# Optimization experiments

Hardware: AMD Instinct MI355X
Metric: run time of the kernel (lower is better)

## Reference

```python
import jax, jax.numpy as jnp
import numpy as np
import math

D_MODEL = 512
NUM_HEADS = 8
HEAD_DIM = D_MODEL // NUM_HEADS
B, S = 4, 2048


def setup_inputs() -> dict:
    key = jax.random.key(0)
    ks = jax.random.split(key, 11)
    scale = 1.0 / math.sqrt(D_MODEL)
    inp = {
        "Q": jax.random.normal(ks[0], (B, S, D_MODEL), jnp.float32),
        "K": jax.random.normal(ks[1], (B, S, D_MODEL), jnp.float32),
        "V": jax.random.normal(ks[2], (B, S, D_MODEL), jnp.float32),
        # causal mask, broadcast over batch and heads: [1,1,S,S]
        "mask": jnp.tril(jnp.ones((S, S), dtype=bool))[None, None],
        "w_q": jax.random.normal(ks[3], (D_MODEL, D_MODEL), jnp.float32) * scale,
        "b_q": jnp.zeros((D_MODEL,), jnp.float32),
        "w_k": jax.random.normal(ks[4], (D_MODEL, D_MODEL), jnp.float32) * scale,
        "b_k": jnp.zeros((D_MODEL,), jnp.float32),
        "w_v": jax.random.normal(ks[5], (D_MODEL, D_MODEL), jnp.float32) * scale,
        "b_v": jnp.zeros((D_MODEL,), jnp.float32),
        "w_o": jax.random.normal(ks[6], (D_MODEL, D_MODEL), jnp.float32) * scale,
        "b_o": jnp.zeros((D_MODEL,), jnp.float32),
    }
    return inp


def _split_heads(x):
    b, s, _ = x.shape
    return x.reshape(b, s, NUM_HEADS, HEAD_DIM).transpose(0, 2, 1, 3)  # [B,H,S,Dh]


def reference(Q, K, V, mask, w_q, b_q, w_k, b_k, w_v, b_v, w_o, b_o):
    # Linear projections (torch Linear: x @ W.T + b)
    q = _split_heads(Q @ w_q.T + b_q)
    k = _split_heads(K @ w_k.T + b_k)
    v = _split_heads(V @ w_v.T + b_v)

    scores = jnp.einsum("bhqd,bhkd->bhqk", q, k) / math.sqrt(HEAD_DIM)
    scores = jnp.where(mask, scores, -jnp.inf)
    attention = jax.nn.softmax(scores, axis=-1)  # [B,H,S,S]
    ctx = jnp.einsum("bhqk,bhkd->bhqd", attention, v)

    b, h, s, dh = ctx.shape
    x = ctx.transpose(0, 2, 1, 3).reshape(b, s, D_MODEL)
    x = x @ w_o.T + b_o
    return (x, attention)
```

## Files before the change

kernel.cpp:

```cpp
#include <hip/hip_runtime.h>


#define BATCH 4
#define SEQ   2048
#define DM    512
#define NH    8
#define DH    64
#define ROWS  (BATCH*SEQ)
#define QT    (SEQ/64)

typedef unsigned short u16;
using bf8   = __attribute__((ext_vector_type(8))) short;
using f32x4 = __attribute__((ext_vector_type(4))) float;

__device__ __forceinline__ u16 f2b(float f) {
    union { float fl; unsigned int i; } v; v.fl = f;
    return (u16)((v.i + 0x7FFFu + ((v.i >> 16) & 1u)) >> 16);
}

__device__ __forceinline__ void proj_body_f32_bf16(
    const float* __restrict__ Xg, const float* __restrict__ W,
    const float* __restrict__ bias, u16* __restrict__ Cg,
    int row0, int col0)
{
    __shared__ u16 Xs[128][40];
    __shared__ u16 Wsh[128][40];
    const int tid  = threadIdx.x;
    const int lane = tid & 63;
    const int w    = tid >> 6;
    const int wm = (w >> 1) * 64, wn = (w & 1) * 64;
    const int lc = lane & 15, lq = lane >> 4;

    const f32x4 fzero = {0.f, 0.f, 0.f, 0.f};
    f32x4 acc[4][4];
    #pragma unroll
    for (int mt = 0; mt < 4; ++mt)
        #pragma unroll
        for (int nt = 0; nt < 4; ++nt) acc[mt][nt] = fzero;

    for (int k0 = 0; k0 < DM; k0 += 32) {
        __syncthreads();
        {
            const int r = tid >> 3, kc = (tid & 7) * 4;
            #pragma unroll
            for (int rr = 0; rr < 4; ++rr) {
                float4 vx = *(const float4*)(Xg + (size_t)(row0 + r + rr*32) * DM + k0 + kc);
                u16 t4[4] = { f2b(vx.x), f2b(vx.y), f2b(vx.z), f2b(vx.w) };
                *(uint2*)&Xs[r + rr*32][kc] = *(uint2*)t4;
                float4 vw = *(const float4*)(W + (size_t)(col0 + r + rr*32) * DM + k0 + kc);
                u16 t5[4] = { f2b(vw.x), f2b(vw.y), f2b(vw.z), f2b(vw.w) };
                *(uint2*)&Wsh[r + rr*32][kc] = *(uint2*)t5;
            }
        }
        __syncthreads();
        bf8 a[4], b[4];
        #pragma unroll
        for (int mt = 0; mt < 4; ++mt) a[mt] = *(const bf8*)&Xs[wm + mt*16 + lc][lq*8];
        #pragma unroll
        for (int nt = 0; nt < 4; ++nt) b[nt] = *(const bf8*)&Wsh[wn + nt*16 + lc][lq*8];
        __builtin_amdgcn_s_setprio(1);
        #pragma unroll
        for (int mt = 0; mt < 4; ++mt)
            #pragma unroll
            for (int nt = 0; nt < 4; ++nt)
                acc[mt][nt] = __builtin_amdgcn_mfma_f32_16x16x32_bf16(a[mt], b[nt], acc[mt][nt], 0, 0, 0);
        __builtin_amdgcn_s_setprio(0);
    }
    #pragma unroll
    for (int nt = 0; nt < 4; ++nt) {
        const int col = col0 + wn + nt*16 + lc;
        const float bv = bias[col];
        #pragma unroll
        for (int mt = 0; mt < 4; ++mt) {
            #pragma unroll
            for (int r = 0; r < 4; ++r) {
                const int row = row0 + wm + mt*16 + lq*4 + r;
                Cg[(size_t)row * DM + col] = f2b(acc[mt][nt][r] + bv);
            }
        }
    }
}

__global__ __launch_bounds__(256) void proj_qkv(
    const float* __restrict__ Q, const float* __restrict__ K, const float* __restrict__ V,
    const float* __restrict__ wq, const float* __restrict__ wk, const float* __restrict__ wv,
    const float* __restrict__ bq, const float* __restrict__ bk, const float* __restrict__ bv,
    u16* __restrict__ qo, u16* __restrict__ ko, u16* __restrict__ vo)
{
    const int z = blockIdx.z;
    const float* X = (z == 0) ? Q : (z == 1) ? K : V;
    const float* W = (z == 0) ? wq : (z == 1) ? wk : wv;
    const float* B = (z == 0) ? bq : (z == 1) ? bk : bv;
    u16*         C = (z == 0) ? qo : (z == 1) ? ko : vo;
    proj_body_f32_bf16(X, W, B, C, blockIdx.y * 128, blockIdx.x * 128);
}

__global__ __launch_bounds__(256) void proj_out(
    const u16* __restrict__ Xg, const float* __restrict__ W,
    const float* __restrict__ bias, float* __restrict__ Cg)
{
    __shared__ u16 Xs[128][40];
    __shared__ u16 Wsh[128][40];
    const int tid  = threadIdx.x;
    const int lane = tid & 63;
    const int w    = tid >> 6;
    const int wm = (w >> 1) * 64, wn = (w & 1) * 64;
    const int lc = lane & 15, lq = lane >> 4;
    const int row0 = blockIdx.y * 128;
    const int col0 = blockIdx.x * 128;

    const f32x4 fzero = {0.f, 0.f, 0.f, 0.f};
    f32x4 acc[4][4];
    #pragma unroll
    for (int mt = 0; mt < 4; ++mt)
        #pragma unroll
        for (int nt = 0; nt < 4; ++nt) acc[mt][nt] = fzero;

    for (int k0 = 0; k0 < DM; k0 += 32) {
        __syncthreads();
        {
            const u16* Xp = Xg;
            const int r = tid >> 2, kc = (tid & 3) * 8;
            #pragma unroll
            for (int rr = 0; rr < 2; ++rr)
                *(bf8*)&Xs[r + rr*64][kc] =
                    *(const bf8*)(Xp + (size_t)(row0 + r + rr*64) * DM + k0 + kc);
        }
        {
            const int r = tid >> 3, kc = (tid & 7) * 4;
            #pragma unroll
            for (int rr = 0; rr < 4; ++rr) {
                float4 vw = *(const float4*)(W + (size_t)(col0 + r + rr*32) * DM + k0 + kc);
                u16 t4[4] = { f2b(vw.x), f2b(vw.y), f2b(vw.z), f2b(vw.w) };
                *(uint2*)&Wsh[r + rr*32][kc] = *(uint2*)t4;
            }
        }
        __syncthreads();
        bf8 a[4], b[4];
        #pragma unroll
        for (int mt = 0; mt < 4; ++mt) a[mt] = *(const bf8*)&Xs[wm + mt*16 + lc][lq*8];
        #pragma unroll
        for (int nt = 0; nt < 4; ++nt) b[nt] = *(const bf8*)&Wsh[wn + nt*16 + lc][lq*8];
        __builtin_amdgcn_s_setprio(1);
        #pragma unroll
        for (int mt = 0; mt < 4; ++mt)
            #pragma unroll
            for (int nt = 0; nt < 4; ++nt)
                acc[mt][nt] = __builtin_amdgcn_mfma_f32_16x16x32_bf16(a[mt], b[nt], acc[mt][nt], 0, 0, 0);
        __builtin_amdgcn_s_setprio(0);
    }
    #pragma unroll
    for (int nt = 0; nt < 4; ++nt) {
        const int col = col0 + wn + nt*16 + lc;
        const float bv = bias[col];
        #pragma unroll
        for (int mt = 0; mt < 4; ++mt) {
            #pragma unroll
            for (int r = 0; r < 4; ++r) {
                const int row = row0 + wm + mt*16 + lq*4 + r;
                Cg[(size_t)row * DM + col] = acc[mt][nt][r] + bv;
            }
        }
    }
}

__global__ __launch_bounds__(256, 3) void attn_fused(
    const u16* __restrict__ q, const u16* __restrict__ k, const u16* __restrict__ v,
    float* __restrict__ att, u16* __restrict__ ctx)
{
    __shared__ u16 Qs[64][72];
    __shared__ u16 Ks[2][64][72];
    __shared__ u16 Vt[64][72];
    __shared__ u16 Ps[64][72];
    __shared__ float Ls[64][17];
    __shared__ float Lv[64];

    const int tid = threadIdx.x, lane = tid & 63, w = tid >> 6;
    const int lc = lane & 15, lq = lane >> 4;

    const int lin = blockIdx.x + 32 * (blockIdx.y + 8 * blockIdx.z);
    const int xcd = lin & 7, c = lin >> 3;
    const int bh  = xcd * 4 + (c >> 5);
    const int qt  = (QT - 1) - (c & 31);
    const int h = bh & 7, b = bh >> 3;

    const size_t base = ((size_t)b * SEQ) * DM + h * DH;
    const size_t attbase = ((size_t)(b * NH + h)) * SEQ * SEQ;
    const int sr = tid >> 3, sc = (tid & 7) * 8;
    const int dv = tid & 63, jg = (tid >> 6) * 16;
    const f32x4 fzero = {0.f, 0.f, 0.f, 0.f};

    #pragma unroll
    for (int rr = 0; rr < 2; ++rr)
        *(bf8*)&Qs[sr + rr*32][sc] =
            *(const bf8*)(q + base + (size_t)(qt*64 + sr + rr*32) * DM + sc);

    float l_p[4];
    #pragma unroll
    for (int r = 0; r < 4; ++r) l_p[r] = 0.f;

    bf8 kr[2];
    #pragma unroll
    for (int rr = 0; rr < 2; ++rr)
        kr[rr] = *(const bf8*)(k + base + (size_t)(sr + rr*32) * DM + sc);
    #pragma unroll
    for (int rr = 0; rr < 2; ++rr)
        *(bf8*)&Ks[0][sr + rr*32][sc] = kr[rr];

    int cur = 0;
    for (int kt = 0; kt <= qt; ++kt) {
        __syncthreads();
        if (kt < qt) {
            #pragma unroll
            for (int rr = 0; rr < 2; ++rr)
                kr[rr] = *(const bf8*)(k + base + (size_t)((kt+1)*64 + sr + rr*32) * DM + sc);
        }
        f32x4 s[4];
        #pragma unroll
        for (int nt = 0; nt < 4; ++nt) s[nt] = fzero;
        __builtin_amdgcn_s_setprio(1);
        #pragma unroll
        for (int ks = 0; ks < 2; ++ks) {
            bf8 a = *(const bf8*)&Qs[w*16 + lc][ks*32 + lq*8];
            #pragma unroll
            for (int nt = 0; nt < 4; ++nt) {
                bf8 bb = *(const bf8*)&Ks[cur][nt*16 + lc][ks*32 + lq*8];
                s[nt] = __builtin_amdgcn_mfma_f32_16x16x32_bf16(a, bb, s[nt], 0, 0, 0);
            }
        }
        __builtin_amdgcn_s_setprio(0);
        const bool diag = (kt == qt);
        #pragma unroll
        for (int r = 0; r < 4; ++r) {
            const int rowl = w*16 + lq*4 + r;
            float e0, e1, e2, e3;
            {
                float x0 = s[0][r] * 0.125f, x1 = s[1][r] * 0.125f;
                float x2 = s[2][r] * 0.125f, x3 = s[3][r] * 0.125f;
                if (diag) {
                    if ( 0*16 + lc > rowl) x0 = -1e30f;
                    if ( 1*16 + lc > rowl) x1 = -1e30f;
                    if ( 2*16 + lc > rowl) x2 = -1e30f;
                    if ( 3*16 + lc > rowl) x3 = -1e30f;
                }
                e0 = __expf(x0); e1 = __expf(x1); e2 = __expf(x2); e3 = __expf(x3);
            }
            l_p[r] += (e0 + e1) + (e2 + e3);
        }
        if (kt < qt) {
            #pragma unroll
            for (int rr = 0; rr < 2; ++rr)
                *(bf8*)&Ks[cur^1][sr + rr*32][sc] = kr[rr];
        }
        cur ^= 1;
    }

    #pragma unroll
    for (int r = 0; r < 4; ++r)
        Ls[w*16 + lq*4 + r][lc] = l_p[r];
    #pragma unroll
    for (int rr = 0; rr < 2; ++rr)
        kr[rr] = *(const bf8*)(k + base + (size_t)(sr + rr*32) * DM + sc);
    u16 tv[16];
    #pragma unroll
    for (int i = 0; i < 16; ++i)
        tv[i] = v[base + (size_t)(jg + i) * DM + dv];
    __syncthreads();
    if (tid < 64) {
        float lf = 0.f;
        #pragma unroll
        for (int t = 0; t < 16; ++t) lf += Ls[tid][t];
        Lv[tid] = 1.0f / lf;
    }
    #pragma unroll
    for (int rr = 0; rr < 2; ++rr)
        *(bf8*)&Ks[0][sr + rr*32][sc] = kr[rr];
    *(bf8*)&Vt[dv][jg]     = *(bf8*)&tv[0];
    *(bf8*)&Vt[dv][jg + 8] = *(bf8*)&tv[8];
    __syncthreads();

    float lvr[4];
    #pragma unroll
    for (int r = 0; r < 4; ++r) lvr[r] = Lv[w*16 + lq*4 + r];

    f32x4 oc[4];
    #pragma unroll
    for (int nt = 0; nt < 4; ++nt) oc[nt] = fzero;

    cur = 0;
    for (int kt = 0; kt <= qt; ++kt) {
        if (kt > 0) __syncthreads();
        if (kt < qt) {
            #pragma unroll
            for (int rr = 0; rr < 2; ++rr)
                kr[rr] = *(const bf8*)(k + base + (size_t)((kt+1)*64 + sr + rr*32) * DM + sc);
            #pragma unroll
            for (int i = 0; i < 16; ++i)
                tv[i] = v[base + (size_t)((kt+1)*64 + jg + i) * DM + dv];
        }
        f32x4 s[4];
        #pragma unroll
        for (int nt = 0; nt < 4; ++nt) s[nt] = fzero;
        __builtin_amdgcn_s_setprio(1);
        #pragma unroll
        for (int ks = 0; ks < 2; ++ks) {
            bf8 a = *(const bf8*)&Qs[w*16 + lc][ks*32 + lq*8];
            #pragma unroll
            for (int nt = 0; nt < 4; ++nt) {
                bf8 bb = *(const bf8*)&Ks[cur][nt*16 + lc][ks*32 + lq*8];
                s[nt] = __builtin_amdgcn_mfma_f32_16x16x32_bf16(a, bb, s[nt], 0, 0, 0);
            }
        }
        __builtin_amdgcn_s_setprio(0);
        const bool diag = (kt == qt);
        #pragma unroll
        for (int nt = 0; nt < 4; ++nt) {
            #pragma unroll
            for (int r = 0; r < 4; ++r) {
                const int rowl = w*16 + lq*4 + r;
                const int coll = nt*16 + lc;
                float p = 0.f;
                if (!diag || coll <= rowl)
                    p = __expf(s[nt][r] * 0.125f) * lvr[r];
                att[attbase + (size_t)(qt*64 + rowl) * SEQ + kt*64 + coll] = p;
                Ps[rowl][coll] = f2b(p);
            }
        }
        __builtin_amdgcn_s_setprio(1);
        #pragma unroll
        for (int ks = 0; ks < 2; ++ks) {
            bf8 a = *(const bf8*)&Ps[w*16 + lc][ks*32 + lq*8];
            #pragma unroll
            for (int nt = 0; nt < 4; ++nt) {
                bf8 bb = *(const bf8*)&Vt[nt*16 + lc][ks*32 + lq*8];
                oc[nt] = __builtin_amdgcn_mfma_f32_16x16x32_bf16(a, bb, oc[nt], 0, 0, 0);
            }
        }
        __builtin_amdgcn_s_setprio(0);
        if (kt < qt) {
            __syncthreads();
            #pragma unroll
            for (int rr = 0; rr < 2; ++rr)
                *(bf8*)&Ks[cur^1][sr + rr*32][sc] = kr[rr];
            *(bf8*)&Vt[dv][jg]     = *(bf8*)&tv[0];
            *(bf8*)&Vt[dv][jg + 8] = *(bf8*)&tv[8];
        }
        cur ^= 1;
    }
    #pragma unroll
    for (int nt = 0; nt < 4; ++nt) {
        #pragma unroll
        for (int r = 0; r < 4; ++r) {
            const int rowl = w*16 + lq*4 + r;
            ctx[((size_t)b * SEQ + qt*64 + rowl) * DM + h*DH + nt*16 + lc] = f2b(oc[nt][r]);
        }
    }
    {
        const int zr = tid >> 2, zc0 = (tid & 3) * 16;
        const float4 z = {0.f, 0.f, 0.f, 0.f};
        for (int ct = qt + 1; ct < QT; ++ct) {
            #pragma unroll
            for (int jj = 0; jj < 4; ++jj)
                *(float4*)(att + attbase + (size_t)(qt*64 + zr) * SEQ + ct*64 + zc0 + jj*4) = z;
        }
    }
}

extern "C" void kernel_launch(void* const* d_in, const int* in_sizes, int n_in,
                              void* d_out, int out_size, void* d_ws, size_t ws_size,
                              hipStream_t stream) {
    const float* Q   = (const float*)d_in[0];
    const float* K   = (const float*)d_in[1];
    const float* V   = (const float*)d_in[2];
    const float* w_q = (const float*)d_in[4];
    const float* b_q = (const float*)d_in[5];
    const float* w_k = (const float*)d_in[6];
    const float* b_k = (const float*)d_in[7];
    const float* w_v = (const float*)d_in[8];
    const float* b_v = (const float*)d_in[9];
    const float* w_o = (const float*)d_in[10];
    const float* b_o = (const float*)d_in[11];

    float* x_out   = (float*)d_out;
    float* att_out = x_out + (size_t)ROWS * DM;

    u16* qw = (u16*)d_ws;
    u16* kw = qw + (size_t)ROWS * DM;
    u16* vw = kw + (size_t)ROWS * DM;
    u16* cw = vw + (size_t)ROWS * DM;

    dim3 pgrid(DM/128, ROWS/128, 3);
    proj_qkv<<<pgrid, 256, 0, stream>>>(Q, K, V, w_q, w_k, w_v,
                                        b_q, b_k, b_v, qw, kw, vw);

    dim3 agrid(QT, NH, BATCH);
    attn_fused<<<agrid, 256, 0, stream>>>(qw, kw, vw, att_out, cw);

    dim3 ogrid(DM/128, ROWS/128);
    proj_out<<<ogrid, 256, 0, stream>>>(cw, w_o, b_o, x_out);
}
```

Measured before the change: 752.3 us.

## Use 128-row query tiles in attention with balanced block scheduling

Each attention block now handles 128 query rows, with each wave owning 32 rows, so every K/V tile loaded into shared memory serves twice as many query rows. The grid becomes 512 linear blocks, and query tiles are paired in reverse and forward order across layers to spread causal work evenly over XCDs. Occupancy drops from 3 to 2 blocks per CU and register and LDS use grow. Masking now tests global row and column for the last two key tiles.

New measurement: 742.7 us. Within noise of the previous version (-1.3%).

```diff
diff --git a/kernel.cpp b/kernel.cpp
--- a/kernel.cpp
+++ b/kernel.cpp
@@ -119,12 +119,11 @@
     for (int k0 = 0; k0 < DM; k0 += 32) {
         __syncthreads();
         {
-            const u16* Xp = Xg;
             const int r = tid >> 2, kc = (tid & 3) * 8;
             #pragma unroll
             for (int rr = 0; rr < 2; ++rr)
                 *(bf8*)&Xs[r + rr*64][kc] =
-                    *(const bf8*)(Xp + (size_t)(row0 + r + rr*64) * DM + k0 + kc);
+                    *(const bf8*)(Xg + (size_t)(row0 + r + rr*64) * DM + k0 + kc);
         }
         {
             const int r = tid >> 3, kc = (tid & 7) * 4;
@@ -164,25 +163,28 @@
     }
 }
 
-__global__ __launch_bounds__(256, 3) void attn_fused(
+__global__ __launch_bounds__(256, 2) void attn_fused(
     const u16* __restrict__ q, const u16* __restrict__ k, const u16* __restrict__ v,
     float* __restrict__ att, u16* __restrict__ ctx)
 {
-    __shared__ u16 Qs[64][72];
+    __shared__ u16 Qs[128][72];
     __shared__ u16 Ks[2][64][72];
     __shared__ u16 Vt[64][72];
-    __shared__ u16 Ps[64][72];
-    __shared__ float Ls[64][17];
-    __shared__ float Lv[64];
+    __shared__ u16 Ps[128][72];
+    __shared__ float Ls[128][17];
+    __shared__ float Lv[128];
 
     const int tid = threadIdx.x, lane = tid & 63, w = tid >> 6;
     const int lc = lane & 15, lq = lane >> 4;
 
-    const int lin = blockIdx.x + 32 * (blockIdx.y + 8 * blockIdx.z);
+    const int lin = blockIdx.x;
     const int xcd = lin & 7, c = lin >> 3;
-    const int bh  = xcd * 4 + (c >> 5);
-    const int qt  = (QT - 1) - (c & 31);
+    const int layer = c >> 5, sub = (c >> 4) & 1, j = c & 15;
+    const int qb = layer ? j : (15 - j);
+    const int bh = xcd * 4 + layer * 2 + sub;
     const int h = bh & 7, b = bh >> 3;
+    const int NT = 2 * qb + 2;
+    const int row0 = qb * 128;
 
     const size_t base = ((size_t)b * SEQ) * DM + h * DH;
     const size_t attbase = ((size_t)(b * NH + h)) * SEQ * SEQ;
@@ -191,13 +193,15 @@
     const f32x4 fzero = {0.f, 0.f, 0.f, 0.f};
 
     #pragma unroll
-    for (int rr = 0; rr < 2; ++rr)
+    for (int rr = 0; rr < 4; ++rr)
         *(bf8*)&Qs[sr + rr*32][sc] =
-            *(const bf8*)(q + base + (size_t)(qt*64 + sr + rr*32) * DM + sc);
-
-    float l_p[4];
-    #pragma unroll
-    for (int r = 0; r < 4; ++r) l_p[r] = 0.f;
+            *(const bf8*)(q + base + (size_t)(row0 + sr + rr*32) * DM + sc);
+
+    float l_p[2][4];
+    #pragma unroll
+    for (int mt = 0; mt < 2; ++mt)
+        #pragma unroll
+        for (int r = 0; r < 4; ++r) l_p[mt][r] = 0.f;
 
     bf8 kr[2];
     #pragma unroll
@@ -208,46 +212,49 @@
         *(bf8*)&Ks[0][sr + rr*32][sc] = kr[rr];
 
     int cur = 0;
-    for (int kt = 0; kt <= qt; ++kt) {
+    for (int kt = 0; kt < NT; ++kt) {
         __syncthreads();
-        if (kt < qt) {
+        if (kt + 1 < NT) {
             #pragma unroll
             for (int rr = 0; rr < 2; ++rr)
                 kr[rr] = *(const bf8*)(k + base + (size_t)((kt+1)*64 + sr + rr*32) * DM + sc);
         }
-        f32x4 s[4];
-        #pragma unroll
-        for (int nt = 0; nt < 4; ++nt) s[nt] = fzero;
+        f32x4 s[2][4];
+        #pragma unroll
+        for (int mt = 0; mt < 2; ++mt)
+            #pragma unroll
+            for (int nt = 0; nt < 4; ++nt) s[mt][nt] = fzero;
         __builtin_amdgcn_s_setprio(1);
         #pragma unroll
         for (int ks = 0; ks < 2; ++ks) {
-            bf8 a = *(const bf8*)&Qs[w*16 + lc][ks*32 + lq*8];
+            bf8 a0 = *(const bf8*)&Qs[w*32 + lc][ks*32 + lq*8];
+            bf8 a1 = *(const bf8*)&Qs[w*32 + 16 + lc][ks*32 + lq*8];
             #pragma unroll
             for (int nt = 0; nt < 4; ++nt) {
                 bf8 bb = *(const bf8*)&Ks[cur][nt*16 + lc][ks*32 + lq*8];
-                s[nt] = __builtin_amdgcn_mfma_f32_16x16x32_bf16(a, bb, s[nt], 0, 0, 0);
+                s[0][nt] = __builtin_amdgcn_mfma_f32_16x16x32_bf16(a0, bb, s[0][nt], 0, 0, 0);
+                s[1][nt] = __builtin_amdgcn_mfma_f32_16x16x32_bf16(a1, bb, s[1][nt], 0, 0, 0);
             }
         }
         __builtin_amdgcn_s_setprio(0);
-        const bool diag = (kt == qt);
-        #pragma unroll
-        for (int r = 0; r < 4; ++r) {
-            const int rowl = w*16 + lq*4 + r;
-            float e0, e1, e2, e3;
-            {
-                float x0 = s[0][r] * 0.125f, x1 = s[1][r] * 0.125f;
-                float x2 = s[2][r] * 0.125f, x3 = s[3][r] * 0.125f;
-                if (diag) {
-                    if ( 0*16 + lc > rowl) x0 = -1e30f;
-                    if ( 1*16 + lc > rowl) x1 = -1e30f;
-                    if ( 2*16 + lc > rowl) x2 = -1e30f;
-                    if ( 3*16 + lc > rowl) x3 = -1e30f;
+        const bool mchk = (kt >= 2*qb);
+        #pragma unroll
+        for (int mt = 0; mt < 2; ++mt) {
+            #pragma unroll
+            for (int r = 0; r < 4; ++r) {
+                const int rowg = row0 + w*32 + mt*16 + lq*4 + r;
+                float e4 = 0.f;
+                #pragma unroll
+                for (int nt = 0; nt < 4; ++nt) {
+                    const int colg = kt*64 + nt*16 + lc;
+                    float e = __expf(s[mt][nt][r] * 0.125f);
+                    if (mchk && colg > rowg) e = 0.f;
+                    e4 += e;
                 }
-                e0 = __expf(x0); e1 = __expf(x1); e2 = __expf(x2); e3 = __expf(x3);
-            }
-            l_p[r] += (e0 + e1) + (e2 + e3);
-        }
-        if (kt < qt) {
+                l_p[mt][r] += e4;
+            }
+        }
+        if (kt + 1 < NT) {
             #pragma unroll
             for (int rr = 0; rr < 2; ++rr)
                 *(bf8*)&Ks[cur^1][sr + rr*32][sc] = kr[rr];
@@ -256,8 +263,10 @@
     }
 
     #pragma unroll
-    for (int r = 0; r < 4; ++r)
-        Ls[w*16 + lq*4 + r][lc] = l_p[r];
+    for (int mt = 0; mt < 2; ++mt)
+        #pragma unroll
+        for (int r = 0; r < 4; ++r)
+            Ls[w*32 + mt*16 + lq*4 + r][lc] = l_p[mt][r];
     #pragma unroll
     for (int rr = 0; rr < 2; ++rr)
         kr[rr] = *(const bf8*)(k + base + (size_t)(sr + rr*32) * DM + sc);
@@ -266,7 +275,7 @@
     for (int i = 0; i < 16; ++i)
         tv[i] = v[base + (size_t)(jg + i) * DM + dv];
     __syncthreads();
-    if (tid < 64) {
+    if (tid < 128) {
         float lf = 0.f;
         #pragma unroll
         for (int t = 0; t < 16; ++t) lf += Ls[tid][t];
@@ -279,18 +288,23 @@
     *(bf8*)&Vt[dv][jg + 8] = *(bf8*)&tv[8];
     __syncthreads();
 
-    float lvr[4];
-    #pragma unroll
-    for (int r = 0; r < 4; ++r) lvr[r] = Lv[w*16 + lq*4 + r];
-
-    f32x4 oc[4];
-    #pragma unroll
-    for (int nt = 0; nt < 4; ++nt) oc[nt] = fzero;
+    float lvr[2][4];
+    #pragma unroll
+    for (int mt = 0; mt < 2; ++mt)
+        #pragma unroll
+        for (int r = 0; r < 4; ++r)
+            lvr[mt][r] = Lv[w*32 + mt*16 + lq*4 + r];
+
+    f32x4 oc[2][4];
+    #pragma unroll
+    for (int mt = 0; mt < 2; ++mt)
+        #pragma unroll
+        for (int nt = 0; nt < 4; ++nt) oc[mt][nt] = fzero;
 
     cur = 0;
-    for (int kt = 0; kt <= qt; ++kt) {
+    for (int kt = 0; kt < NT; ++kt) {
         if (kt > 0) __syncthreads();
-        if (kt < qt) {
+        if (kt + 1 < NT) {
             #pragma unroll
             for (int rr = 0; rr < 2; ++rr)
                 kr[rr] = *(const bf8*)(k + base + (size_t)((kt+1)*64 + sr + rr*32) * DM + sc);
@@ -298,46 +312,54 @@
             for (int i = 0; i < 16; ++i)
                 tv[i] = v[base + (size_t)((kt+1)*64 + jg + i) * DM + dv];
         }
-        f32x4 s[4];
-        #pragma unroll
-        for (int nt = 0; nt < 4; ++nt) s[nt] = fzero;
+        f32x4 s[2][4];
+        #pragma unroll
+        for (int mt = 0; mt < 2; ++mt)
+            #pragma unroll
+            for (int nt = 0; nt < 4; ++nt) s[mt][nt] = fzero;
         __builtin_amdgcn_s_setprio(1);
         #pragma unroll
         for (int ks = 0; ks < 2; ++ks) {
-            bf8 a = *(const bf8*)&Qs[w*16 + lc][ks*32 + lq*8];
+            bf8 a0 = *(const bf8*)&Qs[w*32 + lc][ks*32 + lq*8];
+            bf8 a1 = *(const bf8*)&Qs[w*32 + 16 + lc][ks*32 + lq*8];
             #pragma unroll
             for (int nt = 0; nt < 4; ++nt) {
                 bf8 bb = *(const bf8*)&Ks[cur][nt*16 + lc][ks*32 + lq*8];
-                s[nt] = __builtin_amdgcn_mfma_f32_16x16x32_bf16(a, bb, s[nt], 0, 0, 0);
+                s[0][nt] = __builtin_amdgcn_mfma_f32_16x16x32_bf16(a0, bb, s[0][nt], 0, 0, 0);
+                s[1][nt] = __builtin_amdgcn_mfma_f32_16x16x32_bf16(a1, bb, s[1][nt], 0, 0, 0);
             }
         }
         __builtin_amdgcn_s_setprio(0);
-        const bool diag = (kt == qt);
-        #pragma unroll
-        for (int nt = 0; nt < 4; ++nt) {
-            #pragma unroll
-            for (int r = 0; r < 4; ++r) {
-                const int rowl = w*16 + lq*4 + r;
-                const int coll = nt*16 + lc;
-                float p = 0.f;
-                if (!diag || coll <= rowl)
-                    p = __expf(s[nt][r] * 0.125f) * lvr[r];
-                att[attbase + (size_t)(qt*64 + rowl) * SEQ + kt*64 + coll] = p;
-                Ps[rowl][coll] = f2b(p);
+        const bool mchk = (kt >= 2*qb);
+        #pragma unroll
+        for (int mt = 0; mt < 2; ++mt) {
+            #pragma unroll
+            for (int nt = 0; nt < 4; ++nt) {
+                #pragma unroll
+                for (int r = 0; r < 4; ++r) {
+                    const int rowl = w*32 + mt*16 + lq*4 + r;
+                    const int coll = nt*16 + lc;
+                    float p = __expf(s[mt][nt][r] * 0.125f) * lvr[mt][r];
+                    if (mchk && (kt*64 + coll) > (row0 + rowl)) p = 0.f;
+                    att[attbase + (size_t)(row0 + rowl) * SEQ + kt*64 + coll] = p;
+                    Ps[rowl][coll] = f2b(p);
+                }
             }
         }
         __builtin_amdgcn_s_setprio(1);
         #pragma unroll
         for (int ks = 0; ks < 2; ++ks) {
-            bf8 a = *(const bf8*)&Ps[w*16 + lc][ks*32 + lq*8];
+            bf8 a0 = *(const bf8*)&Ps[w*32 + lc][ks*32 + lq*8];
+            bf8 a1 = *(const bf8*)&Ps[w*32 + 16 + lc][ks*32 + lq*8];
             #pragma unroll
             for (int nt = 0; nt < 4; ++nt) {
                 bf8 bb = *(const bf8*)&Vt[nt*16 + lc][ks*32 + lq*8];
-                oc[nt] = __builtin_amdgcn_mfma_f32_16x16x32_bf16(a, bb, oc[nt], 0, 0, 0);
+                oc[0][nt] = __builtin_amdgcn_mfma_f32_16x16x32_bf16(a0, bb, oc[0][nt], 0, 0, 0);
+                oc[1][nt] = __builtin_amdgcn_mfma_f32_16x16x32_bf16(a1, bb, oc[1][nt], 0, 0, 0);
             }
         }
         __builtin_amdgcn_s_setprio(0);
-        if (kt < qt) {
+        if (kt + 1 < NT) {
             __syncthreads();
             #pragma unroll
             for (int rr = 0; rr < 2; ++rr)
@@ -348,20 +370,23 @@
         cur ^= 1;
     }
     #pragma unroll
-    for (int nt = 0; nt < 4; ++nt) {
-        #pragma unroll
-        for (int r = 0; r < 4; ++r) {
-            const int rowl = w*16 + lq*4 + r;
-            ctx[((size_t)b * SEQ + qt*64 + rowl) * DM + h*DH + nt*16 + lc] = f2b(oc[nt][r]);
+    for (int mt = 0; mt < 2; ++mt) {
+        #pragma unroll
+        for (int nt = 0; nt < 4; ++nt) {
+            #pragma unroll
+            for (int r = 0; r < 4; ++r) {
+                const int rowl = w*32 + mt*16 + lq*4 + r;
+                ctx[((size_t)b * SEQ + row0 + rowl) * DM + h*DH + nt*16 + lc] = f2b(oc[mt][nt][r]);
+            }
         }
     }
     {
-        const int zr = tid >> 2, zc0 = (tid & 3) * 16;
+        const int zr = tid >> 1, zc0 = (tid & 1) * 32;
         const float4 z = {0.f, 0.f, 0.f, 0.f};
-        for (int ct = qt + 1; ct < QT; ++ct) {
-            #pragma unroll
-            for (int jj = 0; jj < 4; ++jj)
-                *(float4*)(att + attbase + (size_t)(qt*64 + zr) * SEQ + ct*64 + zc0 + jj*4) = z;
+        for (int ct = NT; ct < QT; ++ct) {
+            #pragma unroll
+            for (int jj = 0; jj < 8; ++jj)
+                *(float4*)(att + attbase + (size_t)(row0 + zr) * SEQ + ct*64 + zc0 + jj*4) = z;
         }
     }
 }
@@ -393,8 +418,7 @@
     proj_qkv<<<pgrid, 256, 0, stream>>>(Q, K, V, w_q, w_k, w_v,
                                         b_q, b_k, b_v, qw, kw, vw);
 
-    dim3 agrid(QT, NH, BATCH);
-    attn_fused<<<agrid, 256, 0, stream>>>(qw, kw, vw, att_out, cw);
+    attn_fused<<<dim3(512), 256, 0, stream>>>(qw, kw, vw, att_out, cw);
 
     dim3 ogrid(DM/128, ROWS/128);
     proj_out<<<ogrid, 256, 0, stream>>>(cw, w_o, b_o, x_out);
```
